# Kernel tuning notes

Measured on AMD Instinct MI355X. Metric: run time of the kernel, lower is better.

Reference implementation:

```python
import jax, jax.numpy as jnp
import numpy as np

LN_EPS = 1e-5


def _layernorm(h, gamma, beta):
    mu = jnp.mean(h, axis=-1, keepdims=True)
    var = jnp.var(h, axis=-1, keepdims=True)
    return (h - mu) * jax.lax.rsqrt(var + LN_EPS) * gamma + beta


def _simple_attention(q, k, v):
    # DIFFormer 'simple' kernel, num_heads=1: global-Frobenius-normalized q,k,
    # linear attention numerator + uniform component, denominator + N.
    n = q.shape[0]
    qs = q / jnp.linalg.norm(q)            # [N, M]
    ks = k / jnp.linalg.norm(k)            # [N, M]
    kvs = jnp.einsum('lm,ld->md', ks, v)   # [M, D]
    num = jnp.einsum('nm,md->nd', qs, kvs) + jnp.sum(v, axis=0)  # [N, D]
    den = jnp.einsum('nm,m->n', qs, jnp.sum(ks, axis=0)) + jnp.asarray(n, q.dtype)
    return num / den[:, None]


def reference(x, edge_index, W1, b1, Wq, bq, Wk, bk, gamma, beta, alpha, Wr, br, wgt):
    n = x.shape[0]
    row, col = edge_index[0], edge_index[1]
    # symmetric GCN normalization (degree of destination index, as in DIFFormer)
    deg = jax.ops.segment_sum(jnp.ones_like(col, dtype=x.dtype), col, num_segments=n)
    inv_sqrt = jnp.where(deg > 0, 1.0 / jnp.sqrt(deg), 0.0)
    w_edge = inv_sqrt[col] * inv_sqrt[row]  # [E]

    def gcn_conv(v):
        # out[i] = sum_{e: col[e]==i} w[e] * v[row[e]]
        return jax.ops.segment_sum(w_edge[:, None] * v[row], col, num_segments=n)

    def conv(h):
        q = h @ Wq + bq
        k = h @ Wk + bk
        v = h                              # use_weight=False -> value = source input
        return _simple_attention(q, k, v) + gcn_conv(v)

    R = jax.nn.relu(x @ W1 + b1)           # [N, H]
    Ts = [R]
    for _ in range(3):                      # three calls of the SAME shared conv
        Rn = conv(R)
        R = alpha * Rn + (1.0 - alpha) * R  # residual blend
        R = _layernorm(R, gamma, beta)      # shared LayerNorm
        Ts.append(R)

    # multi-head linear readout + learned weighted sum (dropout = identity in eval)
    res = jnp.stack([Ts[i] @ Wr[i] + br[i] for i in range(4)], axis=0)  # [4, N]
    out = jnp.einsum('i,in->n', wgt, res)[:, None]                       # [N, 1]
    return out


def setup_inputs():
    key = jax.random.key(0)
    ks = jax.random.split(key, 8)
    N, E, F_IN, H = 100000, 3200000, 58, 256
    x = jax.random.normal(ks[0], (N, F_IN), dtype=jnp.float32)
    edge_index = jax.random.randint(ks[1], (2, E), 0, N, dtype=jnp.int32)
    s_in = 1.0 / np.sqrt(F_IN)
    s_h = 1.0 / np.sqrt(H)
    return {
        'x': x,
        'edge_index': edge_index,
        'W1': jax.random.normal(ks[2], (F_IN, H), dtype=jnp.float32) * s_in,
        'b1': jnp.zeros((H,), jnp.float32),
        'Wq': jax.random.normal(ks[3], (H, H), dtype=jnp.float32) * s_h,
        'bq': jnp.zeros((H,), jnp.float32),
        'Wk': jax.random.normal(ks[4], (H, H), dtype=jnp.float32) * s_h,
        'bk': jnp.zeros((H,), jnp.float32),
        'gamma': jnp.ones((H,), jnp.float32),
        'beta': jnp.zeros((H,), jnp.float32),
        'alpha': jnp.float32(0.5),
        'Wr': jax.random.normal(ks[5], (4, H), dtype=jnp.float32) * s_h,
        'br': jnp.zeros((4,), jnp.float32),
        'wgt': jnp.array([0.5, 0.5, 0.5, 0.5], jnp.float32),
    }
```

## Files before the change

### kernel.cpp

```cpp
#include <hip/hip_runtime.h>

#define H 256
#define FIN 58
#define LN_EPS 1e-5f
#define EPB 8192
#define SBW 11

typedef __bf16 bf16x8 __attribute__((ext_vector_type(8)));
typedef float f32x16 __attribute__((ext_vector_type(16)));
typedef float f32x2 __attribute__((ext_vector_type(2)));

union FragU {
  ushort u[8];
  bf16x8 v;
};


__device__ __forceinline__ float wave_sum(float v) {
#pragma unroll
  for (int off = 1; off < 64; off <<= 1) v += __shfl_xor(v, off, 64);
  return v;
}

__device__ __forceinline__ float half_sum(float v) {
#pragma unroll
  for (int off = 1; off < 32; off <<= 1) v += __shfl_xor(v, off, 64);
  return v;
}

__device__ __forceinline__ float block_sum(float v, volatile float* red) {
  const int tid = threadIdx.x;
  v = wave_sum(v);
  __syncthreads();
  if ((tid & 63) == 0) red[tid >> 6] = v;
  __syncthreads();
  return red[0] + red[1] + red[2] + red[3];
}

__device__ __forceinline__ ushort f2bf(float f) {
  unsigned u = __float_as_uint(f);
  unsigned r = (u + 0x7FFFu + ((u >> 16) & 1u)) >> 16;
  return (ushort)r;
}

__device__ __forceinline__ float bf2f(ushort u) {
  return __uint_as_float((unsigned)u << 16);
}

#if __has_builtin(__builtin_amdgcn_cvt_pk_fp8_f32) && __has_builtin(__builtin_amdgcn_cvt_pk_f32_fp8)
__device__ __forceinline__ unsigned pack_fp8x4(float a, float b, float c, float d) {
  int v = 0;
  v = __builtin_amdgcn_cvt_pk_fp8_f32(a, b, v, false);
  v = __builtin_amdgcn_cvt_pk_fp8_f32(c, d, v, true);
  return (unsigned)v;
}
__device__ __forceinline__ void unpack_fp8x2_acc(f32x2& lo, f32x2& hi, unsigned v) {
  lo += __builtin_amdgcn_cvt_pk_f32_fp8((int)v, false);
  hi += __builtin_amdgcn_cvt_pk_f32_fp8((int)v, true);
}
#else
__device__ __forceinline__ unsigned char f2e4m3_1(float f) {
  unsigned u = __float_as_uint(f);
  unsigned s = (u >> 31) << 7;
  float a = fabsf(f);
  if (a >= 448.0f) return (unsigned char)(s | 0x7E);
  if (a < 0.0009765625f) return (unsigned char)s;
  int e;
  float m = frexpf(a, &e);
  int E = e - 1 + 7;
  if (E >= 1) {
    int mm = (int)rintf((m * 2.0f - 1.0f) * 8.0f);
    if (mm == 8) { mm = 0; E++; }
    return (unsigned char)(s | (E << 3) | mm);
  }
  int mm = (int)rintf(a * 512.0f);
  if (mm > 7) return (unsigned char)(s | (1 << 3));
  return (unsigned char)(s | mm);
}
__device__ __forceinline__ unsigned pack_fp8x4(float a, float b, float c, float d) {
  return (unsigned)f2e4m3_1(a) | ((unsigned)f2e4m3_1(b) << 8) |
         ((unsigned)f2e4m3_1(c) << 16) | ((unsigned)f2e4m3_1(d) << 24);
}
__device__ __forceinline__ float e4m3f_1(unsigned v) {
  int s = (v >> 7) & 1, E = (v >> 3) & 15, m = v & 7;
  float mag = E ? ldexpf(1.0f + m * 0.125f, E - 7) : ldexpf((float)m, -9);
  return s ? -mag : mag;
}
__device__ __forceinline__ void unpack_fp8x2_acc(f32x2& lo, f32x2& hi, unsigned v) {
  lo[0] += e4m3f_1(v & 255);
  lo[1] += e4m3f_1((v >> 8) & 255);
  hi[0] += e4m3f_1((v >> 16) & 255);
  hi[1] += e4m3f_1(v >> 24);
}
#endif


__global__ __launch_bounds__(512) void k_b1(const int* __restrict__ row,
                                            const int* __restrict__ col,
                                            unsigned* __restrict__ breg,
                                            int* __restrict__ gcnt,
                                            int cap2, int E, int nsb) {
  __shared__ unsigned stage[EPB];
  __shared__ int lh[65], lbase[65], lcur[64], gclaim[64];
  const int tid = threadIdx.x;
  const int e0 = blockIdx.x * EPB;
  const int cnt = min(EPB, E - e0);
  if (tid < 64) lh[tid] = 0;
  __syncthreads();
  for (int i = tid; i < cnt; i += 512) atomicAdd(&lh[col[e0 + i] >> SBW], 1);
  __syncthreads();
  if (tid == 0) {
    int acc = 0;
    for (int b = 0; b < nsb; b++) { lbase[b] = acc; acc += lh[b]; }
    lbase[nsb] = acc;
  }
  __syncthreads();
  if (tid < nsb) {
    gclaim[tid] = atomicAdd(&gcnt[tid], lh[tid]);
    lcur[tid] = lbase[tid];
  }
  __syncthreads();
  for (int i = tid; i < cnt; i += 512) {
    int c = col[e0 + i];
    int b = c >> SBW;
    int s = atomicAdd(&lcur[b], 1);
    stage[s] = ((unsigned)row[e0 + i] << SBW) | (unsigned)(c & ((1 << SBW) - 1));
  }
  __syncthreads();
  for (int i = tid; i < cnt; i += 512) {
    int lo = 0, hi = nsb;
    while (hi - lo > 1) {
      int mid = (lo + hi) >> 1;
      if (lbase[mid] <= i) lo = mid; else hi = mid;
    }
    int off = gclaim[lo] + (i - lbase[lo]);
    if (off < cap2) breg[(size_t)lo * cap2 + off] = stage[i];
  }
}

__global__ __launch_bounds__(512) void k_degB2(const unsigned* __restrict__ breg,
                                               const int* __restrict__ gcnt, int cap2,
                                               int* __restrict__ deg,
                                               float* __restrict__ invs, int N) {
  __shared__ int lcnt[1 << SBW];
  const int b = blockIdx.x, tid = threadIdx.x, base = b << SBW;
  for (int i = tid; i < (1 << SBW); i += 512) lcnt[i] = 0;
  __syncthreads();
  const int cnt = min(gcnt[b], cap2);
  const unsigned* p = breg + (size_t)b * cap2;
  for (int i = tid; i < cnt; i += 512) atomicAdd(&lcnt[p[i] & ((1 << SBW) - 1)], 1);
  __syncthreads();
  for (int i = tid; i < (1 << SBW); i += 512) {
    int d = base + i;
    if (d < N) {
      int c = lcnt[i];
      deg[d] = c;
      invs[d] = (c > 0) ? (1.0f / sqrtf((float)c)) : 0.0f;
    }
  }
}

__global__ __launch_bounds__(512) void k_b2(const unsigned* __restrict__ breg,
                                            const int* __restrict__ gcnt, int cap2,
                                            int* __restrict__ offs16,
                                            const int* __restrict__ bsum,
                                            int* __restrict__ eb, int N) {
  __shared__ int loffs[1 << SBW];
  __shared__ int lcur[1 << SBW];
  const int b = blockIdx.x, tid = threadIdx.x, base = b << SBW;
  for (int i = tid; i < (1 << SBW); i += 512) {
    int d = base + i;
    if (d < N) {
      int o = offs16[d] + bsum[d >> 10];
      loffs[i] = o;
      offs16[d] = o;
    } else {
      loffs[i] = 0;
    }
    lcur[i] = 0;
  }
  __syncthreads();
  const int cnt = min(gcnt[b], cap2);
  const unsigned* p = breg + (size_t)b * cap2;
  for (int i = tid; i < cnt; i += 512) {
    unsigned rc = p[i];
    int lc = rc & ((1 << SBW) - 1);
    int slot = atomicAdd(&lcur[lc], 1);
    eb[loffs[lc] + slot] = (int)(rc >> SBW);
  }
  __syncthreads();
  for (int i = tid; i < (1 << SBW); i += 512) {
    int d = base + i;
    if (d < N) {
      int c = lcur[i];
      int pad = (c + 15) & ~15;
      int o = loffs[i];
      for (int j = c; j < pad; j++) eb[o + j] = N;
    }
  }
}

__global__ __launch_bounds__(1024) void k_scan1(const int* __restrict__ deg,
                                                int* __restrict__ offs16,
                                                int* __restrict__ bsum, int N) {
  __shared__ int buf[1024];
  const int tid = threadIdx.x;
  const int gid = blockIdx.x * 1024 + tid;
  int v = (gid < N) ? ((deg[gid] + 15) & ~15) : 0;
  buf[tid] = v;
  __syncthreads();
  for (int off = 1; off < 1024; off <<= 1) {
    int x = (tid >= off) ? buf[tid - off] : 0;
    __syncthreads();
    buf[tid] += x;
    __syncthreads();
  }
  if (gid < N) offs16[gid] = buf[tid] - v;
  if (tid == 1023) bsum[blockIdx.x] = buf[1023];
}

__global__ __launch_bounds__(1024) void k_scan2(int* __restrict__ bsum, int nb) {
  __shared__ int buf[1024];
  const int tid = threadIdx.x;
  int v = (tid < nb) ? bsum[tid] : 0;
  buf[tid] = v;
  __syncthreads();
  for (int off = 1; off < 1024; off <<= 1) {
    int x = (tid >= off) ? buf[tid - off] : 0;
    __syncthreads();
    buf[tid] += x;
    __syncthreads();
  }
  if (tid < nb) bsum[tid] = buf[tid] - v;
}

__global__ void k_prep(const float* __restrict__ Wq, const float* __restrict__ Wk,
                       const float* __restrict__ bq, const float* __restrict__ bk,
                       float* __restrict__ P, float* __restrict__ Q, float* __restrict__ K2,
                       float* __restrict__ pb, float* __restrict__ qb,
                       float* __restrict__ wb, float* __restrict__ kb,
                       float* __restrict__ sconst) {
  __shared__ float red[4];
  const int b = blockIdx.x, tid = threadIdx.x;
  if (b < 768) {
    const int f = b & 255, which = b >> 8;
    const float* A = (which == 2) ? Wk : Wq;
    const float* Bm = (which == 1) ? Wq : Wk;
    float acc = 0.0f;
    for (int m = 0; m < H; m++) acc = fmaf(A[f * H + m], Bm[tid * H + m], acc);
    float* D = (which == 0) ? P : ((which == 1) ? Q : K2);
    D[f * H + tid] = acc;
  } else {
    float a1 = 0, a2 = 0, a3 = 0, a4 = 0;
    for (int m = 0; m < H; m++) {
      float wqv = Wq[tid * H + m], wkv = Wk[tid * H + m];
      a1 = fmaf(wqv, bk[m], a1);
      a2 = fmaf(wqv, bq[m], a2);
      a3 = fmaf(wkv, bq[m], a3);
      a4 = fmaf(wkv, bk[m], a4);
    }
    pb[tid] = a1; qb[tid] = a2; wb[tid] = a3; kb[tid] = a4;
    float c0 = block_sum(bq[tid] * bk[tid], red);
    float c1 = block_sum(bq[tid] * bq[tid], red);
    float c2 = block_sum(bk[tid] * bk[tid], red);
    if (tid == 0) { sconst[0] = c0; sconst[1] = c1; sconst[2] = c2; }
  }
}

__global__ void k_fc1(const float* __restrict__ x, const float* __restrict__ W1,
                      const float* __restrict__ b1, const float* __restrict__ Wr,
                      const float* __restrict__ br, const float* __restrict__ wgt,
                      ushort* __restrict__ R0, float* __restrict__ out, int N) {
  __shared__ __align__(16) float lx[16 * FIN];
  __shared__ float red2[4][16];
  const int tid = threadIdx.x;
  const int n0 = blockIdx.x * 16;
  for (int idx = tid; idx < 16 * FIN / 4; idx += 256)
    ((float4*)lx)[idx] = ((const float4*)(x + (size_t)n0 * FIN))[idx];
  __syncthreads();
  float acc[16];
  const float bias = b1[tid];
#pragma unroll
  for (int r = 0; r < 16; r++) acc[r] = bias;
  for (int f = 0; f < FIN; f++) {
    float wv = W1[f * H + tid];
#pragma unroll
    for (int r = 0; r < 16; r++) acc[r] = fmaf(lx[r * FIN + f], wv, acc[r]);
  }
  const float wr0 = Wr[tid];
#pragma unroll
  for (int r = 0; r < 16; r++) {
    acc[r] = fmaxf(acc[r], 0.0f);
    int n = n0 + r;
    if (n < N) R0[(size_t)n * H + tid] = f2bf(acc[r]);
  }
#pragma unroll
  for (int r = 0; r < 16; r++) {
    float s = wave_sum(acc[r] * wr0);
    if ((tid & 63) == 0) red2[tid >> 6][r] = s;
  }
  __syncthreads();
  if (tid < 16) {
    int n = n0 + tid;
    if (n < N)
      out[n] = wgt[0] * (red2[0][tid] + red2[1][tid] + red2[2][tid] + red2[3][tid] + br[0]);
  }
}

__global__ __launch_bounds__(512, 2) void k_Gm(const ushort* __restrict__ Rb,
                                               const float* __restrict__ invs,
                                               ushort* __restrict__ Gslab,
                                               unsigned* __restrict__ Rf8,
                                               float* __restrict__ csl, int N) {
  __shared__ ushort sbT[2][256 * 32];
  const int tid = threadIdx.x;
  const int lane = tid & 63;
  const int wid = tid >> 6;
  const int wrow = (wid & 1) * 128;
  const int wcol = (wid >> 1) * 64;
  const int l31 = lane & 31;
  const int lhi = lane >> 5;

  const int TC = (N + 31) >> 5;
  const int cbase = TC >> 8;
  const int crem = TC & 255;
  const int b = blockIdx.x;
  const int startc = b * cbase + min(b, crem);
  const int nch = cbase + (b < crem ? 1 : 0);
  const int rowbase = startc * 32;

  const int rp = tid >> 5;
  const int fg = tid & 31;
  const int k2 = rp * 2;

  f32x16 acc[4][2];
#pragma unroll
  for (int s = 0; s < 4; s++)
#pragma unroll
    for (int t = 0; t < 2; t++)
#pragma unroll
      for (int e = 0; e < 16; e++) acc[s][t][e] = 0.0f;

  float cs[8];
#pragma unroll
  for (int i = 0; i < 8; i++) cs[i] = 0.0f;

  int4 la, lb;
  float sc0, sc1;

  auto load_chunk = [&](int ch) {
    int g0 = rowbase + ch * 32 + k2;
    const int4* s0 = (const int4*)(Rb + (size_t)g0 * H + fg * 8);
    const int4* s1 = (const int4*)(Rb + (size_t)(g0 + 1) * H + fg * 8);
    la = (g0 < N) ? s0[0] : make_int4(0, 0, 0, 0);
    lb = (g0 + 1 < N) ? s1[0] : make_int4(0, 0, 0, 0);
    sc0 = (g0 < N) ? invs[g0] : 0.0f;
    sc1 = (g0 + 1 < N) ? invs[g0 + 1] : 0.0f;
  };

  auto write_chunk = [&](int ch, int buf) {
    int g0 = rowbase + ch * 32 + k2;
    const ushort* pa = (const ushort*)&la;
    const ushort* pbu = (const ushort*)&lb;
    const int blk = (k2 & 24) ^ ((fg & 3) << 3);
    uint* dst = (uint*)sbT[buf];
#pragma unroll
    for (int i = 0; i < 8; i++) {
      float av = bf2f(pa[i]), bv = bf2f(pbu[i]);
      cs[i] += av + bv;
      unsigned val = (unsigned)pa[i] | ((unsigned)pbu[i] << 16);
      int f = fg * 8 + i;
      dst[f * 16 + ((blk + (k2 & 7)) >> 1)] = val;
    }
    if (g0 < N) {
      unsigned w0 = pack_fp8x4(bf2f(pa[0]) * sc0, bf2f(pa[1]) * sc0,
                               bf2f(pa[2]) * sc0, bf2f(pa[3]) * sc0);
      unsigned w1 = pack_fp8x4(bf2f(pa[4]) * sc0, bf2f(pa[5]) * sc0,
                               bf2f(pa[6]) * sc0, bf2f(pa[7]) * sc0);
      *(uint2*)&Rf8[(size_t)g0 * 64 + fg * 2] = make_uint2(w0, w1);
    }
    if (g0 + 1 < N) {
      unsigned w0 = pack_fp8x4(bf2f(pbu[0]) * sc1, bf2f(pbu[1]) * sc1,
                               bf2f(pbu[2]) * sc1, bf2f(pbu[3]) * sc1);
      unsigned w1 = pack_fp8x4(bf2f(pbu[4]) * sc1, bf2f(pbu[5]) * sc1,
                               bf2f(pbu[6]) * sc1, bf2f(pbu[7]) * sc1);
      *(uint2*)&Rf8[(size_t)(g0 + 1) * 64 + fg * 2] = make_uint2(w0, w1);
    }
  };

  auto compute = [&](int buf) {
    const ushort* bp = sbT[buf];
#pragma unroll
    for (int ks = 0; ks < 2; ks++) {
      const int kb = ks * 16 + lhi * 8;
      FragU fr[6];
#pragma unroll
      for (int s = 0; s < 6; s++) {
        const int cb = (s < 4) ? (wrow + 32 * s + l31) : (wcol + 32 * (s - 4) + l31);
        const int off = cb * 32 + (kb ^ (((cb >> 3) & 3) << 3));
        *(int4*)fr[s].u = *(const int4*)(bp + off);
      }
#pragma unroll
      for (int s = 0; s < 4; s++)
#pragma unroll
        for (int t = 0; t < 2; t++)
          acc[s][t] = __builtin_amdgcn_mfma_f32_32x32x16_bf16(fr[s].v, fr[4 + t].v,
                                                              acc[s][t], 0, 0, 0);
    }
  };

  load_chunk(0);
  write_chunk(0, 0);
  __syncthreads();
  int cur = 0;
  for (int c = 0; c < nch; c++) {
    if (c + 1 < nch) load_chunk(c + 1);
    compute(cur);
    if (c + 1 < nch) write_chunk(c + 1, cur ^ 1);
    __syncthreads();
    cur ^= 1;
  }

  ushort* Gs = Gslab + (size_t)b * 65536;
#pragma unroll
  for (int s = 0; s < 4; s++)
#pragma unroll
    for (int t = 0; t < 2; t++) {
      const int n0c = wcol + 32 * t + l31;
#pragma unroll
      for (int r = 0; r < 16; r++) {
        const int row = wrow + 32 * s + (r & 3) + 8 * (r >> 2) + 4 * lhi;
        Gs[row * 256 + n0c] = f2bf(acc[s][t][r]);
      }
    }

  __syncthreads();
  float* fl = (float*)sbT;
#pragma unroll
  for (int i = 0; i < 8; i++) fl[rp * 256 + fg * 8 + i] = cs[i];
  __syncthreads();
  if (tid < 256) {
    float v = 0.0f;
    for (int j = 0; j < 16; j++) v += fl[j * 256 + tid];
    csl[(size_t)b * 256 + tid] = v;
  }
}

__global__ void k_Gr(const ushort* __restrict__ Gslab, const float* __restrict__ csl,
                     const float* __restrict__ Q, const float* __restrict__ K2,
                     float* __restrict__ G, float* __restrict__ vsum,
                     float2* __restrict__ spart, int nslab) {
  __shared__ float red[4];
  const int b = blockIdx.x, t = threadIdx.x;
  const int i = b * 256 + t;
  float s0 = 0, s1 = 0, s2 = 0, s3 = 0;
  int j = 0;
  for (; j + 3 < nslab; j += 4) {
    s0 += bf2f(Gslab[(size_t)j * 65536 + i]);
    s1 += bf2f(Gslab[(size_t)(j + 1) * 65536 + i]);
    s2 += bf2f(Gslab[(size_t)(j + 2) * 65536 + i]);
    s3 += bf2f(Gslab[(size_t)(j + 3) * 65536 + i]);
  }
  float s = s0 + s1 + s2 + s3;
  for (; j < nslab; j++) s += bf2f(Gslab[(size_t)j * 65536 + i]);
  G[i] = s;
  float dq = block_sum(s * Q[i], red);
  float dk = block_sum(s * K2[i], red);
  if (t == 0) spart[b] = make_float2(dq, dk);
  float v = 0.0f;
  for (int u = t; u < nslab; u += 256) v += csl[(size_t)u * 256 + b];
  v = block_sum(v, red);
  if (t == 0) vsum[b] = v;
}

__global__ void k_small(const float* __restrict__ G, const float* __restrict__ vsum,
                        const float* __restrict__ P, const float* __restrict__ pb,
                        const float* __restrict__ wb, const float* __restrict__ sconst,
                        const float* __restrict__ qb, const float* __restrict__ kbv,
                        const float2* __restrict__ spart,
                        ushort* __restrict__ Mt, float* __restrict__ cvec,
                        float* __restrict__ dvec, float* __restrict__ scal, int N) {
  __shared__ float red[4];
  const int b = blockIdx.x, tid = threadIdx.x;
  if (b < 256) {
    float acc = 0.0f;
    for (int m = 0; m < H; m++) acc = fmaf(P[b * H + m], G[m * H + tid], acc);
    Mt[(size_t)tid * H + b] = f2bf(acc + pb[b] * vsum[tid]);
  } else if (b == 256) {
    float acc = 0.0f;
    for (int f = 0; f < H; f++) acc = fmaf(wb[f], G[f * H + tid], acc);
    cvec[tid] = acc + sconst[0] * vsum[tid];
  } else if (b == 257) {
    float acc = 0.0f;
    for (int m = 0; m < H; m++) acc = fmaf(P[tid * H + m], vsum[m], acc);
    dvec[tid] = acc + (float)N * pb[tid];
  } else {
    float2 sp = spart[tid];
    float dq = block_sum(sp.x, red);
    float dk = block_sum(sp.y, red);
    float s1 = block_sum(qb[tid] * vsum[tid], red);
    float s2 = block_sum(kbv[tid] * vsum[tid], red);
    float s3 = block_sum(wb[tid] * vsum[tid], red);
    if (tid == 0) {
      float sq = dq + 2.0f * s1 + (float)N * sconst[1];
      float sk = dk + 2.0f * s2 + (float)N * sconst[2];
      scal[2] = 1.0f / (sqrtf(sq) * sqrtf(sk));
      scal[3] = s3 + (float)N * sconst[0];
    }
  }
}

__global__ __launch_bounds__(256, 4) void k_C(
    const ushort* __restrict__ Rb, ushort* __restrict__ Rnext,
    const ushort* __restrict__ Mt, const unsigned* __restrict__ Rf8,
    const int* __restrict__ eb, const float* __restrict__ invs,
    const float* __restrict__ cvec, const float* __restrict__ dvec,
    const float* __restrict__ vsum, const float* __restrict__ scal,
    const int* __restrict__ offs16, const int* __restrict__ deg,
    const float* __restrict__ alphap, const float* __restrict__ gamma,
    const float* __restrict__ beta, const float* __restrict__ Wr,
    const float* __restrict__ br, const float* __restrict__ wgt,
    float* __restrict__ out, int N, int layer, int last) {
  __shared__ __align__(16) ushort lnum[32 * 256];
  const int tid = threadIdx.x, lane = tid & 63, wv = tid >> 6;
  const int half = lane >> 5, hl = lane & 31;
  const int d0 = hl * 8;
  const int nb0 = blockIdx.x * 32;

  {
    f32x16 a0, a1;
#pragma unroll
    for (int e = 0; e < 16; e++) { a0[e] = 0.0f; a1[e] = 0.0f; }
    const int wcol = wv * 64;
    const ushort* aptr = Rb + (size_t)(nb0 + hl) * H;
    const ushort* bptr0 = Mt + (size_t)(wcol + hl) * H;
    const ushort* bptr1 = Mt + (size_t)(wcol + 32 + hl) * H;
    for (int kc = 0; kc < 16; kc++) {
      const int kb = kc * 16 + half * 8;
      FragU fa, fb0, fb1;
      *(int4*)fa.u = *(const int4*)(aptr + kb);
      *(int4*)fb0.u = *(const int4*)(bptr0 + kb);
      *(int4*)fb1.u = *(const int4*)(bptr1 + kb);
      a0 = __builtin_amdgcn_mfma_f32_32x32x16_bf16(fa.v, fb0.v, a0, 0, 0, 0);
      a1 = __builtin_amdgcn_mfma_f32_32x32x16_bf16(fa.v, fb1.v, a1, 0, 0, 0);
    }
#pragma unroll
    for (int r = 0; r < 16; r++) {
      const int row = (r & 3) + 8 * (r >> 2) + 4 * half;
      lnum[row * 256 + wcol + hl] = f2bf(a0[r]);
      lnum[row * 256 + wcol + 32 + hl] = f2bf(a1[r]);
    }
  }
  __syncthreads();

  const float invn = scal[2], denc = scal[3];
  const float al = alphap[0], om = 1.0f - al;
  const float4 dvA = *(const float4*)&dvec[d0];
  const float4 dvB = *(const float4*)&dvec[d0 + 4];
  const float4 cvA = *(const float4*)&cvec[d0];
  const float4 cvB = *(const float4*)&cvec[d0 + 4];
  const float4 vsA = *(const float4*)&vsum[d0];
  const float4 vsB = *(const float4*)&vsum[d0 + 4];
  const float4 gmA = *(const float4*)&gamma[d0];
  const float4 gmB = *(const float4*)&gamma[d0 + 4];
  const float4 btA = *(const float4*)&beta[d0];
  const float4 btB = *(const float4*)&beta[d0 + 4];
  const float4 wrA = *(const float4*)&Wr[layer * H + d0];
  const float4 wrB = *(const float4*)&Wr[layer * H + d0 + 4];
  const float wl = wgt[layer], bl = br[layer];

  for (int r = 0; r < 4; r++) {
    const int lr = wv * 8 + r * 2 + half;
    const int n = nb0 + lr;
    const bool valid = n < N;
    const int ns = valid ? n : 0;

    const int4 rv = *(const int4*)&Rb[(size_t)ns * H + d0];
    const ushort* rp = (const ushort*)&rv;
    const int4 nv = *(const int4*)&lnum[lr * 256 + d0];
    const ushort* np = (const ushort*)&nv;
    float old[8], num[8];
#pragma unroll
    for (int j = 0; j < 8; j++) { old[j] = bf2f(rp[j]); num[j] = bf2f(np[j]); }

    float p = old[0] * dvA.x + old[1] * dvA.y + old[2] * dvA.z + old[3] * dvA.w +
              old[4] * dvB.x + old[5] * dvB.y + old[6] * dvB.z + old[7] * dvB.w;
    p = half_sum(p);
    const float rden = 1.0f / ((p + denc) * invn + (float)N);

    f32x2 a01 = {0.f, 0.f}, a23 = {0.f, 0.f}, a45 = {0.f, 0.f}, a67 = {0.f, 0.f};
    const int st = offs16[ns];
    const int nbch = valid ? ((deg[ns] + 15) >> 4) : 0;
    const int4* pe = (const int4*)(eb + st);
    const int woff = hl * 2;
    for (int b = 0; b < nbch; b++, pe += 4) {
      int4 q0 = pe[0], q1 = pe[1], q2 = pe[2], q3 = pe[3];
      const int srcs[16] = {q0.x, q0.y, q0.z, q0.w, q1.x, q1.y, q1.z, q1.w,
                            q2.x, q2.y, q2.z, q2.w, q3.x, q3.y, q3.z, q3.w};
      uint2 g[16];
#pragma unroll
      for (int i = 0; i < 16; i++)
        g[i] = *(const uint2*)&Rf8[((size_t)srcs[i] << 6) + woff];
#pragma unroll
      for (int i = 0; i < 16; i++) {
        unpack_fp8x2_acc(a01, a23, g[i].x);
        unpack_fp8x2_acc(a45, a67, g[i].y);
      }
    }
    const float sn = invs[ns];
    float ag[8] = {a01[0] * sn, a01[1] * sn, a23[0] * sn, a23[1] * sn,
                   a45[0] * sn, a45[1] * sn, a67[0] * sn, a67[1] * sn};

    const float cva[8] = {cvA.x, cvA.y, cvA.z, cvA.w, cvB.x, cvB.y, cvB.z, cvB.w};
    const float vsa[8] = {vsA.x, vsA.y, vsA.z, vsA.w, vsB.x, vsB.y, vsB.z, vsB.w};
    float hv[8];
#pragma unroll
    for (int j = 0; j < 8; j++)
      hv[j] = al * (((num[j] + cva[j]) * invn + vsa[j]) * rden + ag[j]) + om * old[j];

    float s = 0.0f, s2 = 0.0f;
#pragma unroll
    for (int j = 0; j < 8; j++) { s += hv[j]; s2 += hv[j] * hv[j]; }
    s = half_sum(s);
    s2 = half_sum(s2);
    const float mu = s * (1.0f / H);
    const float var = s2 * (1.0f / H) - mu * mu;
    const float rs = rsqrtf(var + LN_EPS);

    const float gma[8] = {gmA.x, gmA.y, gmA.z, gmA.w, gmB.x, gmB.y, gmB.z, gmB.w};
    const float bta[8] = {btA.x, btA.y, btA.z, btA.w, btB.x, btB.y, btB.z, btB.w};
    const float wra[8] = {wrA.x, wrA.y, wrA.z, wrA.w, wrB.x, wrB.y, wrB.z, wrB.w};
    float y[8], rp2 = 0.0f;
    ushort yo[8];
#pragma unroll
    for (int j = 0; j < 8; j++) {
      y[j] = (hv[j] - mu) * rs * gma[j] + bta[j];
      yo[j] = f2bf(y[j]);
      rp2 += y[j] * wra[j];
    }
    if (!last && valid) *(int4*)&Rnext[(size_t)n * H + d0] = *(int4*)yo;
    rp2 = half_sum(rp2);
    if (hl == 0 && valid) out[n] += wl * (rp2 + bl);
  }
}


extern "C" void kernel_launch(void* const* d_in, const int* in_sizes, int n_in,
                              void* d_out, int out_size, void* d_ws, size_t ws_size,
                              hipStream_t stream) {
  const float* x = (const float*)d_in[0];
  const int* ei = (const int*)d_in[1];
  const float* W1 = (const float*)d_in[2];
  const float* b1 = (const float*)d_in[3];
  const float* Wq = (const float*)d_in[4];
  const float* bq = (const float*)d_in[5];
  const float* Wk = (const float*)d_in[6];
  const float* bk = (const float*)d_in[7];
  const float* gamma = (const float*)d_in[8];
  const float* beta = (const float*)d_in[9];
  const float* alphap = (const float*)d_in[10];
  const float* Wr = (const float*)d_in[11];
  const float* br = (const float*)d_in[12];
  const float* wgt = (const float*)d_in[13];
  float* out = (float*)d_out;

  const int N = in_sizes[0] / FIN;
  const int E = in_sizes[1] / 2;
  const int* row = ei;
  const int* col = ei + E;

  char* w = (char*)d_ws;
  auto alloc = [&](size_t bytes) -> char* {
    char* p = w;
    w += (bytes + 255) & ~(size_t)255;
    return p;
  };
  const size_t RB = (size_t)(N + 128) * H * sizeof(ushort);
  ushort* Rb0 = (ushort*)alloc(RB);
  ushort* Rb1 = (ushort*)alloc(RB);
  ushort* Gslab = (ushort*)alloc((size_t)256 * 65536 * sizeof(ushort));
  unsigned* Rf8 = (unsigned*)alloc((size_t)(N + 1) * 64 * sizeof(unsigned));
  ushort* Mt = (ushort*)alloc(H * H * sizeof(ushort));
  float* G = (float*)alloc(H * H * sizeof(float));
  float* vsum = (float*)alloc(1024);
  float* scal = (float*)alloc(256);
  float* cvec = (float*)alloc(1024);
  float* dvec = (float*)alloc(1024);
  float* P = (float*)alloc(H * H * sizeof(float));
  float* Q = (float*)alloc(H * H * sizeof(float));
  float* K2 = (float*)alloc(H * H * sizeof(float));
  float* pb = (float*)alloc(1024);
  float* qb = (float*)alloc(1024);
  float* wb = (float*)alloc(1024);
  float* kb = (float*)alloc(1024);
  float* sconst = (float*)alloc(256);
  int* deg = (int*)alloc((size_t)N * 4);
  float* invs = (float*)alloc((size_t)N * 4);
  int* offs16 = (int*)alloc((size_t)(N + 1) * 4);
  int* bsum = (int*)alloc(1024 * 4);
  int* gcnt = (int*)alloc(64 * 4);
  const int nbG = 256;
  float* csl = (float*)alloc((size_t)nbG * 256 * sizeof(float));
  float2* spart = (float2*)alloc(256 * sizeof(float2));
  size_t EPAD = (size_t)E + 16 * (size_t)N;
  EPAD = (EPAD + 3) & ~(size_t)3;
  int* eb = (int*)alloc(EPAD * sizeof(int));

  const int NSB = (N + (1 << SBW) - 1) >> SBW;
  int cap2 = (E / (NSB > 0 ? NSB : 1)) * 2 + 4096;
  cap2 = (cap2 + 3) & ~3;
  unsigned* breg = (unsigned*)Rb1;

  hipMemsetAsync(gcnt, 0, 64 * 4, stream);
  hipMemsetAsync(Rf8 + (size_t)N * 64, 0, 64 * sizeof(unsigned), stream);

  const int nblk = (N + 1023) / 1024;
  const int nbB1 = (E + EPB - 1) / EPB;
  k_b1<<<nbB1, 512, 0, stream>>>(row, col, breg, gcnt, cap2, E, NSB);
  k_degB2<<<NSB, 512, 0, stream>>>(breg, gcnt, cap2, deg, invs, N);
  k_scan1<<<nblk, 1024, 0, stream>>>(deg, offs16, bsum, N);
  k_scan2<<<1, 1024, 0, stream>>>(bsum, nblk);
  k_b2<<<NSB, 512, 0, stream>>>(breg, gcnt, cap2, offs16, bsum, eb, N);
  k_prep<<<769, 256, 0, stream>>>(Wq, Wk, bq, bk, P, Q, K2, pb, qb, wb, kb, sconst);
  const int gRows16 = (N + 15) / 16;
  k_fc1<<<gRows16, 256, 0, stream>>>(x, W1, b1, Wr, br, wgt, Rb0, out, N);

  const int gRows32 = (N + 31) / 32;
  ushort* Rc = Rb0;
  ushort* Rn = Rb1;
  for (int it = 1; it <= 3; ++it) {
    k_Gm<<<nbG, 512, 0, stream>>>(Rc, invs, Gslab, Rf8, csl, N);
    k_Gr<<<256, 256, 0, stream>>>(Gslab, csl, Q, K2, G, vsum, spart, nbG);
    k_small<<<259, 256, 0, stream>>>(G, vsum, P, pb, wb, sconst, qb, kb, spart,
                                     Mt, cvec, dvec, scal, N);
    k_C<<<gRows32, 256, 0, stream>>>(Rc, Rn, Mt, Rf8, eb, invs, cvec, dvec, vsum, scal,
                                     offs16, deg, alphap, gamma, beta, Wr, br, wgt, out,
                                     N, it, (it == 3) ? 1 : 0);
    ushort* t = Rc; Rc = Rn; Rn = t;
  }
}
```

Before: 1.030 ms.

## Run edge gather and denominator before the block barrier to overlap with MFMA

```diff
diff --git a/kernel.cpp b/kernel.cpp
--- a/kernel.cpp
+++ b/kernel.cpp
@@ -551,12 +551,58 @@
       lnum[row * 256 + wcol + 32 + hl] = f2bf(a1[r]);
     }
   }
-  __syncthreads();
 
   const float invn = scal[2], denc = scal[3];
   const float al = alphap[0], om = 1.0f - al;
-  const float4 dvA = *(const float4*)&dvec[d0];
-  const float4 dvB = *(const float4*)&dvec[d0 + 4];
+
+  float den[4];
+  float ag[4][8];
+  {
+    const float4 dvA = *(const float4*)&dvec[d0];
+    const float4 dvB = *(const float4*)&dvec[d0 + 4];
+#pragma unroll
+    for (int r = 0; r < 4; r++) {
+      const int lr = wv * 8 + r * 2 + half;
+      const int n = nb0 + lr;
+      const bool valid = n < N;
+      const int ns = valid ? n : 0;
+
+      const int4 rv = *(const int4*)&Rb[(size_t)ns * H + d0];
+      const ushort* rp = (const ushort*)&rv;
+      float p = bf2f(rp[0]) * dvA.x + bf2f(rp[1]) * dvA.y + bf2f(rp[2]) * dvA.z +
+                bf2f(rp[3]) * dvA.w + bf2f(rp[4]) * dvB.x + bf2f(rp[5]) * dvB.y +
+                bf2f(rp[6]) * dvB.z + bf2f(rp[7]) * dvB.w;
+      p = half_sum(p);
+      den[r] = 1.0f / ((p + denc) * invn + (float)N);
+
+      f32x2 a01 = {0.f, 0.f}, a23 = {0.f, 0.f}, a45 = {0.f, 0.f}, a67 = {0.f, 0.f};
+      const int st = offs16[ns];
+      const int nbch = valid ? ((deg[ns] + 15) >> 4) : 0;
+      const int4* pe = (const int4*)(eb + st);
+      const int woff = hl * 2;
+      for (int b = 0; b < nbch; b++, pe += 4) {
+        int4 q0 = pe[0], q1 = pe[1], q2 = pe[2], q3 = pe[3];
+        const int srcs[16] = {q0.x, q0.y, q0.z, q0.w, q1.x, q1.y, q1.z, q1.w,
+                              q2.x, q2.y, q2.z, q2.w, q3.x, q3.y, q3.z, q3.w};
+        uint2 g[16];
+#pragma unroll
+        for (int i = 0; i < 16; i++)
+          g[i] = *(const uint2*)&Rf8[((size_t)srcs[i] << 6) + woff];
+#pragma unroll
+        for (int i = 0; i < 16; i++) {
+          unpack_fp8x2_acc(a01, a23, g[i].x);
+          unpack_fp8x2_acc(a45, a67, g[i].y);
+        }
+      }
+      const float sn = invs[ns];
+      ag[r][0] = a01[0] * sn; ag[r][1] = a01[1] * sn;
+      ag[r][2] = a23[0] * sn; ag[r][3] = a23[1] * sn;
+      ag[r][4] = a45[0] * sn; ag[r][5] = a45[1] * sn;
+      ag[r][6] = a67[0] * sn; ag[r][7] = a67[1] * sn;
+    }
+  }
+  __syncthreads();
+
   const float4 cvA = *(const float4*)&cvec[d0];
   const float4 cvB = *(const float4*)&cvec[d0 + 4];
   const float4 vsA = *(const float4*)&vsum[d0];
@@ -568,7 +614,13 @@
   const float4 wrA = *(const float4*)&Wr[layer * H + d0];
   const float4 wrB = *(const float4*)&Wr[layer * H + d0 + 4];
   const float wl = wgt[layer], bl = br[layer];
-
+  const float cva[8] = {cvA.x, cvA.y, cvA.z, cvA.w, cvB.x, cvB.y, cvB.z, cvB.w};
+  const float vsa[8] = {vsA.x, vsA.y, vsA.z, vsA.w, vsB.x, vsB.y, vsB.z, vsB.w};
+  const float gma[8] = {gmA.x, gmA.y, gmA.z, gmA.w, gmB.x, gmB.y, gmB.z, gmB.w};
+  const float bta[8] = {btA.x, btA.y, btA.z, btA.w, btB.x, btB.y, btB.z, btB.w};
+  const float wra[8] = {wrA.x, wrA.y, wrA.z, wrA.w, wrB.x, wrB.y, wrB.z, wrB.w};
+
+#pragma unroll
   for (int r = 0; r < 4; r++) {
     const int lr = wv * 8 + r * 2 + half;
     const int n = nb0 + lr;
@@ -579,44 +631,13 @@
     const ushort* rp = (const ushort*)&rv;
     const int4 nv = *(const int4*)&lnum[lr * 256 + d0];
     const ushort* np = (const ushort*)&nv;
-    float old[8], num[8];
-#pragma unroll
-    for (int j = 0; j < 8; j++) { old[j] = bf2f(rp[j]); num[j] = bf2f(np[j]); }
-
-    float p = old[0] * dvA.x + old[1] * dvA.y + old[2] * dvA.z + old[3] * dvA.w +
-              old[4] * dvB.x + old[5] * dvB.y + old[6] * dvB.z + old[7] * dvB.w;
-    p = half_sum(p);
-    const float rden = 1.0f / ((p + denc) * invn + (float)N);
-
-    f32x2 a01 = {0.f, 0.f}, a23 = {0.f, 0.f}, a45 = {0.f, 0.f}, a67 = {0.f, 0.f};
-    const int st = offs16[ns];
-    const int nbch = valid ? ((deg[ns] + 15) >> 4) : 0;
-    const int4* pe = (const int4*)(eb + st);
-    const int woff = hl * 2;
-    for (int b = 0; b < nbch; b++, pe += 4) {
-      int4 q0 = pe[0], q1 = pe[1], q2 = pe[2], q3 = pe[3];
-      const int srcs[16] = {q0.x, q0.y, q0.z, q0.w, q1.x, q1.y, q1.z, q1.w,
-                            q2.x, q2.y, q2.z, q2.w, q3.x, q3.y, q3.z, q3.w};
-      uint2 g[16];
-#pragma unroll
-      for (int i = 0; i < 16; i++)
-        g[i] = *(const uint2*)&Rf8[((size_t)srcs[i] << 6) + woff];
-#pragma unroll
-      for (int i = 0; i < 16; i++) {
-        unpack_fp8x2_acc(a01, a23, g[i].x);
-        unpack_fp8x2_acc(a45, a67, g[i].y);
-      }
-    }
-    const float sn = invs[ns];
-    float ag[8] = {a01[0] * sn, a01[1] * sn, a23[0] * sn, a23[1] * sn,
-                   a45[0] * sn, a45[1] * sn, a67[0] * sn, a67[1] * sn};
-
-    const float cva[8] = {cvA.x, cvA.y, cvA.z, cvA.w, cvB.x, cvB.y, cvB.z, cvB.w};
-    const float vsa[8] = {vsA.x, vsA.y, vsA.z, vsA.w, vsB.x, vsB.y, vsB.z, vsB.w};
+    const float rden = den[r];
+
     float hv[8];
 #pragma unroll
     for (int j = 0; j < 8; j++)
-      hv[j] = al * (((num[j] + cva[j]) * invn + vsa[j]) * rden + ag[j]) + om * old[j];
+      hv[j] = al * (((bf2f(np[j]) + cva[j]) * invn + vsa[j]) * rden + ag[r][j]) +
+              om * bf2f(rp[j]);
 
     float s = 0.0f, s2 = 0.0f;
 #pragma unroll
@@ -627,9 +648,6 @@
     const float var = s2 * (1.0f / H) - mu * mu;
     const float rs = rsqrtf(var + LN_EPS);
 
-    const float gma[8] = {gmA.x, gmA.y, gmA.z, gmA.w, gmB.x, gmB.y, gmB.z, gmB.w};
-    const float bta[8] = {btA.x, btA.y, btA.z, btA.w, btB.x, btB.y, btB.z, btB.w};
-    const float wra[8] = {wrA.x, wrA.y, wrA.z, wrA.w, wrB.x, wrB.y, wrB.z, wrB.w};
     float y[8], rp2 = 0.0f;
     ushort yo[8];
 #pragma unroll
```

New measurement: 1.036 ms. No clear change (+0.5%).
